# Optimization experiments

Hardware: AMD Instinct MI355X
Metric: run time of the kernel (lower is better)

Reference implementation:

```python
import jax, jax.numpy as jnp
import numpy as np

N_EXAMPLES = 32768
N_CLASSES = 1000
N_BINS = 15


def setup_inputs() -> dict:
    key = jax.random.key(0)
    k1, k2 = jax.random.split(key)
    # logits as produced by the (frozen) base model
    logits = jax.random.normal(k1, (N_EXAMPLES, N_CLASSES), dtype=jnp.float32) * 3.0
    # per-bin accuracy estimates from histogram_binning(); -1.0 marks an empty bin
    histogram = jax.random.uniform(k2, (N_BINS,), dtype=jnp.float32)
    histogram = histogram.at[0].set(-1.0)
    return {"logits": logits, "histogram": histogram}


def reference(logits, histogram):
    """Vectorized histogram-binning calibration.

    Returns (sm_calib [N,C], valid_flag [N], predictions [N]) matching
    forward() -> get_calibrated_softmax_vector() of the torch module.
    """
    n_bins = histogram.shape[0]
    n_classes = logits.shape[1]

    sm = jax.nn.softmax(logits, axis=1)                      # [N, C]
    conf = jnp.max(sm, axis=1)                               # argmax softmax score
    pred = jnp.argmax(sm, axis=1)                            # [N]

    # torch.histc bins are (lower, upper]; index = ceil(conf * n_bins) - 1
    bin_idx = jnp.clip(jnp.ceil(conf * n_bins).astype(jnp.int32) - 1, 0, n_bins - 1)
    h = histogram[bin_idx]                                   # [N] bin accuracy lookup
    valid_flag = (h != -1.0).astype(jnp.float32)
    # empty bin (-1) -> fall back to raw confidence
    est = jnp.where(h == -1.0, conf, h)                      # [N]

    onehot = jax.nn.one_hot(pred, n_classes, dtype=sm.dtype)  # [N, C]
    masked = sm * (1.0 - onehot)                              # zero out argmax entry
    denom = jnp.sum(masked, axis=1, keepdims=True)            # mass of the rest
    rescaled = (1.0 - est)[:, None] * masked / denom
    rescaled = rescaled * (1.0 - onehot) + est[:, None] * onehot
    # final renormalization (sums to 1 up to fp error, kept for faithfulness)
    sm_calib = rescaled / jnp.sum(rescaled, axis=1, keepdims=True)
    return sm_calib, valid_flag, pred
```

## Files before the change

kernel.cpp:

```cpp
#include <hip/hip_runtime.h>
#include <math.h>


constexpr int N_EX    = 32768;
constexpr int N_CLS   = 1000;
constexpr int N_BINS  = 15;
constexpr int C4      = N_CLS / 4;

typedef float vf4 __attribute__((ext_vector_type(4)));

__global__ __launch_bounds__(256) void hb_calib_kernel(
    const float* __restrict__ logits,
    const float* __restrict__ hist,
    float* __restrict__ out)
{
    const int wave = threadIdx.x >> 6;
    const int lane = threadIdx.x & 63;
    const int row  = blockIdx.x * 4 + wave;

    const vf4* lrow = reinterpret_cast<const vf4*>(logits + (size_t)row * N_CLS);

    vf4 v[4];
    #pragma unroll
    for (int r = 0; r < 4; ++r) {
        const int q  = lane + 64 * r;
        const int ql = (q < C4) ? q : (C4 - 1);
        v[r] = lrow[ql];
    }

    float lmax = -INFINITY;
    int   lidx = N_CLS;
    #pragma unroll
    for (int r = 0; r < 4; ++r) {
        const int q = lane + 64 * r;
        if (q < C4) {
            #pragma unroll
            for (int t = 0; t < 4; ++t) {
                const int col = 4 * q + t;
                const float x = v[r][t];
                if (x > lmax) { lmax = x; lidx = col; }
            }
        }
    }

    float m   = lmax;
    int   mix = lidx;
    #pragma unroll
    for (int off = 32; off >= 1; off >>= 1) {
        const float ov = __shfl_xor(m, off);
        const int   oi = __shfl_xor(mix, off);
        if (ov > m || (ov == m && oi < mix)) { m = ov; mix = oi; }
    }

    float lsum = 0.0f;
    #pragma unroll
    for (int r = 0; r < 4; ++r) {
        const int q = lane + 64 * r;
        if (q < C4) {
            #pragma unroll
            for (int t = 0; t < 4; ++t) {
                const float e = __expf(v[r][t] - m);
                v[r][t] = e;
                lsum += e;
            }
        }
    }
    float s = lsum;
    #pragma unroll
    for (int off = 32; off >= 1; off >>= 1) s += __shfl_xor(s, off);

    const float srest = s - 1.0f;
    const float conf  = 1.0f / s;

    int bin = (int)ceilf(conf * (float)N_BINS) - 1;
    bin = bin < 0 ? 0 : (bin > N_BINS - 1 ? N_BINS - 1 : bin);
    const float h     = hist[bin];
    const float valid = (h != -1.0f) ? 1.0f : 0.0f;
    const float est   = (h == -1.0f) ? conf : h;

    const float scale = (1.0f - est) / srest;

    vf4* orow = reinterpret_cast<vf4*>(out + (size_t)row * N_CLS);
    #pragma unroll
    for (int r = 0; r < 4; ++r) {
        const int q = lane + 64 * r;
        if (q < C4) {
            vf4 o;
            #pragma unroll
            for (int t = 0; t < 4; ++t) {
                const int col = 4 * q + t;
                o[t] = (col == mix) ? est : v[r][t] * scale;
            }
            __builtin_nontemporal_store(o, &orow[q]);
        }
    }

    if (lane == 0) {
        const size_t base = (size_t)N_EX * N_CLS;
        __builtin_nontemporal_store(valid, &out[base + row]);
        __builtin_nontemporal_store((float)mix, &out[base + N_EX + row]);
    }
}

extern "C" void kernel_launch(void* const* d_in, const int* in_sizes, int n_in,
                              void* d_out, int out_size, void* d_ws, size_t ws_size,
                              hipStream_t stream) {
    const float* logits = (const float*)d_in[0];
    const float* hist   = (const float*)d_in[1];
    float* out          = (float*)d_out;

    const int rows_per_block = 4;
    const int grid = (N_EX + rows_per_block - 1) / rows_per_block;
    hb_calib_kernel<<<grid, 256, 0, stream>>>(logits, hist, out);
}
```

Measured before the change: 44.52 us.

## Process four rows per wave with double-buffered register prefetch

Shrinks the grid from 8192 blocks to 2048 and has each wave handle four rows strided by the total wave count. Two register buffers are used so the next row's logits load is issued before the current row is reduced and written, overlapping memory latency with compute. This cuts block launch overhead and keeps more loads in flight per wave, at the cost of higher register use and fewer resident waves.

```diff
diff --git a/kernel.cpp b/kernel.cpp
--- a/kernel.cpp
+++ b/kernel.cpp
@@ -7,29 +7,29 @@
 constexpr int N_BINS  = 15;
 constexpr int C4      = N_CLS / 4;
 
+constexpr int NBLK       = 2048;
+constexpr int WAVES_TOT  = NBLK * 4;
+constexpr int ROWS_PER_W = N_EX / WAVES_TOT;
+
 typedef float vf4 __attribute__((ext_vector_type(4)));
 
-__global__ __launch_bounds__(256) void hb_calib_kernel(
-    const float* __restrict__ logits,
-    const float* __restrict__ hist,
-    float* __restrict__ out)
+__device__ __forceinline__ void load_row(vf4 (&v)[4], const float* __restrict__ logits,
+                                         int row, int lane)
 {
-    const int wave = threadIdx.x >> 6;
-    const int lane = threadIdx.x & 63;
-    const int row  = blockIdx.x * 4 + wave;
-
     const vf4* lrow = reinterpret_cast<const vf4*>(logits + (size_t)row * N_CLS);
-
-    vf4 v[4];
     #pragma unroll
     for (int r = 0; r < 4; ++r) {
         const int q  = lane + 64 * r;
         const int ql = (q < C4) ? q : (C4 - 1);
         v[r] = lrow[ql];
     }
+}
 
-    float lmax = -INFINITY;
-    int   lidx = N_CLS;
+__device__ __forceinline__ void proc_row(vf4 (&v)[4], const float* __restrict__ hist,
+                                         float* __restrict__ out, int row, int lane)
+{
+    float m = -INFINITY;
+    int   mix = N_CLS;
     #pragma unroll
     for (int r = 0; r < 4; ++r) {
         const int q = lane + 64 * r;
@@ -38,21 +38,17 @@
             for (int t = 0; t < 4; ++t) {
                 const int col = 4 * q + t;
                 const float x = v[r][t];
-                if (x > lmax) { lmax = x; lidx = col; }
+                if (x > m) { m = x; mix = col; }
             }
         }
     }
-
-    float m   = lmax;
-    int   mix = lidx;
     #pragma unroll
     for (int off = 32; off >= 1; off >>= 1) {
         const float ov = __shfl_xor(m, off);
         const int   oi = __shfl_xor(mix, off);
         if (ov > m || (ov == m && oi < mix)) { m = ov; mix = oi; }
     }
-
-    float lsum = 0.0f;
+    float s = 0.0f;
     #pragma unroll
     for (int r = 0; r < 4; ++r) {
         const int q = lane + 64 * r;
@@ -61,24 +57,20 @@
             for (int t = 0; t < 4; ++t) {
                 const float e = __expf(v[r][t] - m);
                 v[r][t] = e;
-                lsum += e;
+                s += e;
             }
         }
     }
-    float s = lsum;
     #pragma unroll
     for (int off = 32; off >= 1; off >>= 1) s += __shfl_xor(s, off);
 
-    const float srest = s - 1.0f;
-    const float conf  = 1.0f / s;
-
+    const float conf = 1.0f / s;
     int bin = (int)ceilf(conf * (float)N_BINS) - 1;
     bin = bin < 0 ? 0 : (bin > N_BINS - 1 ? N_BINS - 1 : bin);
     const float h     = hist[bin];
     const float valid = (h != -1.0f) ? 1.0f : 0.0f;
     const float est   = (h == -1.0f) ? conf : h;
-
-    const float scale = (1.0f - est) / srest;
+    const float scale = (1.0f - est) / (s - 1.0f);
 
     vf4* orow = reinterpret_cast<vf4*>(out + (size_t)row * N_CLS);
     #pragma unroll
@@ -94,12 +86,36 @@
             __builtin_nontemporal_store(o, &orow[q]);
         }
     }
-
     if (lane == 0) {
         const size_t base = (size_t)N_EX * N_CLS;
         __builtin_nontemporal_store(valid, &out[base + row]);
         __builtin_nontemporal_store((float)mix, &out[base + N_EX + row]);
     }
+}
+
+__global__ __launch_bounds__(256) void hb_calib_kernel(
+    const float* __restrict__ logits,
+    const float* __restrict__ hist,
+    float* __restrict__ out)
+{
+    const int wave = threadIdx.x >> 6;
+    const int lane = threadIdx.x & 63;
+    const int gw   = blockIdx.x * 4 + wave;
+
+    const int r0 = gw;
+    const int r1 = gw + WAVES_TOT;
+    const int r2 = gw + 2 * WAVES_TOT;
+    const int r3 = gw + 3 * WAVES_TOT;
+
+    vf4 A[4], B[4];
+    load_row(A, logits, r0, lane);
+    load_row(B, logits, r1, lane);
+    proc_row(A, hist, out, r0, lane);
+    load_row(A, logits, r2, lane);
+    proc_row(B, hist, out, r1, lane);
+    load_row(B, logits, r3, lane);
+    proc_row(A, hist, out, r2, lane);
+    proc_row(B, hist, out, r3, lane);
 }
 
 extern "C" void kernel_launch(void* const* d_in, const int* in_sizes, int n_in,
@@ -109,7 +125,5 @@
     const float* hist   = (const float*)d_in[1];
     float* out          = (float*)d_out;
 
-    const int rows_per_block = 4;
-    const int grid = (N_EX + rows_per_block - 1) / rows_per_block;
-    hb_calib_kernel<<<grid, 256, 0, stream>>>(logits, hist, out);
+    hb_calib_kernel<<<NBLK, 256, 0, stream>>>(logits, hist, out);
 }
```

Result: slower. 46.13 us (+3.6%).
